# Optimization experiments

Measured on AMD Instinct MI355X. Metric: run time of the kernel, lower is better.

Reference implementation:

```python
import jax, jax.numpy as jnp
import numpy as np

EMBED = 1024
HEADS = 16
HEAD_DIM = EMBED // HEADS


def setup_inputs() -> dict:
    key = jax.random.key(0)
    k1, k2, k3 = jax.random.split(key, 3)
    hidden_states = jax.random.normal(k1, (2, 2048, EMBED), dtype=jnp.float32)
    # Conv1D weights are stored (nx, nf): y = x @ W + b
    c_attn_w = jax.random.normal(k2, (EMBED, 3 * EMBED), dtype=jnp.float32) * 0.02
    c_attn_b = jnp.zeros((3 * EMBED,), dtype=jnp.float32)
    c_proj_w = jax.random.normal(k3, (EMBED, EMBED), dtype=jnp.float32) * 0.02
    c_proj_b = jnp.zeros((EMBED,), dtype=jnp.float32)
    return {
        "hidden_states": hidden_states,
        "c_attn_w": c_attn_w,
        "c_attn_b": c_attn_b,
        "c_proj_w": c_proj_w,
        "c_proj_b": c_proj_b,
    }


def reference(hidden_states, c_attn_w, c_attn_b, c_proj_w, c_proj_b):
    B, S, E = hidden_states.shape
    H, D = HEADS, HEAD_DIM
    fused = hidden_states @ c_attn_w + c_attn_b  # [B,S,3E]
    q, k, v = jnp.split(fused, 3, axis=-1)
    # split heads -> [B,H,S,D]
    q = q.reshape(B, S, H, D).transpose(0, 2, 1, 3)
    k = k.reshape(B, S, H, D).transpose(0, 2, 1, 3)
    v = v.reshape(B, S, H, D).transpose(0, 2, 1, 3)
    scores = jnp.einsum("bhqd,bhkd->bhqk", q, k) / jnp.sqrt(jnp.float32(D))
    probs = jax.nn.softmax(scores, axis=-1)  # NOTE: no causal mask in source
    attn = jnp.einsum("bhqk,bhkd->bhqd", probs, v)
    out = attn.transpose(0, 2, 1, 3).reshape(B, S, E)
    return out @ c_proj_w + c_proj_b
```

## Files before the change

kernel.cpp:

```cpp
#include <hip/hip_runtime.h>
#include <hip/hip_bf16.h>
#include <cstdint>
#include <cstddef>

#define E_ 1024
#define H_ 16
#define D_ 64
#define B_ 2
#define S_ 2048
#define T_ 4096
#define NQ_ 3072

typedef __bf16 bf16_t;
typedef bf16_t bf16x8 __attribute__((ext_vector_type(8)));
typedef float f32x4 __attribute__((ext_vector_type(4)));

static __device__ __forceinline__ unsigned short f2bf(float f) {
    __hip_bfloat16 h = __float2bfloat16(f);
    return __builtin_bit_cast(unsigned short, h);
}
static __device__ __forceinline__ unsigned pack2(float a, float b) {
    return (unsigned)f2bf(a) | ((unsigned)f2bf(b) << 16);
}
static __device__ __forceinline__ bf16x8 ld_frag(const unsigned short* p) {
    uint4 u = *reinterpret_cast<const uint4*>(p);
    return __builtin_bit_cast(bf16x8, u);
}
static __device__ __forceinline__ void cp16(unsigned short* lds, const unsigned short* g) {
    __builtin_amdgcn_global_load_lds(
        (const __attribute__((address_space(1))) unsigned int*)g,
        (__attribute__((address_space(3))) unsigned int*)lds, 16, 0, 0);
}
static __device__ __forceinline__ f32x4 mfma16(bf16x8 a, bf16x8 b, f32x4 c) {
    return __builtin_amdgcn_mfma_f32_16x16x32_bf16(a, b, c, 0, 0, 0);
}
static __device__ __forceinline__ unsigned pack2_trunc(unsigned a_bits, unsigned b_bits) {
    return __builtin_amdgcn_perm(b_bits, a_bits, 0x07060302u);
}


__global__ __launch_bounds__(256) void k_cvt(const float* __restrict__ in,
                                             unsigned short* __restrict__ out, int n) {
    int i = (blockIdx.x * 256 + threadIdx.x) * 4;
    if (i < n) {
        float4 v = *reinterpret_cast<const float4*>(in + i);
        int tok = i >> 10, e = i & 1023;
        size_t off = ((size_t)(tok >> 7) * 32 + (e >> 5)) * 4096 + (tok & 127) * 32 + (e & 31);
        uint2 o;
        o.x = pack2(v.x, v.y);
        o.y = pack2(v.z, v.w);
        *reinterpret_cast<uint2*>(out + off) = o;
    }
}

__global__ __launch_bounds__(256) void k_wt(const float* __restrict__ in,
                                            unsigned short* __restrict__ out, int K, int N) {
    __shared__ float t[32][33];
    int n0 = blockIdx.x * 32, k0 = blockIdx.y * 32;
    int tx = threadIdx.x, ty = threadIdx.y;
    for (int j = 0; j < 4; j++) {
        int r = ty + j * 8;
        t[r][tx] = in[(size_t)(k0 + r) * N + n0 + tx];
    }
    __syncthreads();
    int nkt = K >> 5;
    for (int j = 0; j < 4; j++) {
        int r = ty + j * 8;
        int nn = n0 + r;
        size_t off = ((size_t)(nn >> 7) * nkt + (k0 >> 5)) * 4096 + (nn & 127) * 32 + tx;
        out[off] = f2bf(t[tx][r]);
    }
}

template <bool TR>
static __device__ __forceinline__ void gemm_tile_128(
    const unsigned short* __restrict__ At,
    const unsigned short* __restrict__ Bt,
    int nkt, int m0, int n0,
    unsigned short* As, unsigned short* Bs,
    f32x4 acc[4][4])
{
    const int t = threadIdx.x;
    const int w = t >> 6, lane = t & 63, lr = lane & 15, lq = lane >> 4;
    const int wm = (w >> 1) * 64, wn = (w & 1) * 64;
    for (int mt = 0; mt < 4; mt++)
        for (int nt = 0; nt < 4; nt++)
            acc[mt][nt] = (f32x4){0.f, 0.f, 0.f, 0.f};

    const unsigned short* ag = At + (size_t)(m0 >> 7) * nkt * 4096 + t * 8;
    const unsigned short* bg = Bt + (size_t)(n0 >> 7) * nkt * 4096 + t * 8;

    for (int kt = 0; kt < nkt; kt++) {
        __syncthreads();
        cp16(&As[t * 8], ag);          cp16(&As[(t + 256) * 8], ag + 2048);
        cp16(&Bs[t * 8], bg);          cp16(&Bs[(t + 256) * 8], bg + 2048);
        ag += 4096; bg += 4096;
        __syncthreads();
        bf16x8 af[4], bfr[4];
        for (int mt = 0; mt < 4; mt++) af[mt]  = ld_frag(&As[(wm + mt * 16 + lr) * 32 + lq * 8]);
        for (int nt = 0; nt < 4; nt++) bfr[nt] = ld_frag(&Bs[(wn + nt * 16 + lr) * 32 + lq * 8]);
        for (int mt = 0; mt < 4; mt++)
            for (int nt = 0; nt < 4; nt++)
                acc[mt][nt] = TR ? mfma16(bfr[nt], af[mt], acc[mt][nt])
                                 : mfma16(af[mt], bfr[nt], acc[mt][nt]);
    }
}

__global__ __launch_bounds__(256) void k_qkv(
    const unsigned short* __restrict__ Ab, const unsigned short* __restrict__ Wt,
    const float* __restrict__ bias,
    unsigned short* __restrict__ Qb, unsigned short* __restrict__ Kimg,
    unsigned short* __restrict__ Vimg)
{
    __shared__ __attribute__((aligned(16))) unsigned short As[128 * 32];
    __shared__ __attribute__((aligned(16))) unsigned short Bs[128 * 32];
    f32x4 acc[4][4];
    int m0 = blockIdx.x * 128, n0 = blockIdx.y * 128;
    int sector = (n0 >> 10);
    if (sector == 2) gemm_tile_128<false>(Ab, Wt, E_ / 32, m0, n0, As, Bs, acc);
    else             gemm_tile_128<true >(Ab, Wt, E_ / 32, m0, n0, As, Bs, acc);

    int t = threadIdx.x, w = t >> 6, lane = t & 63, lr = lane & 15, lq = lane >> 4;
    int wm = (w >> 1) * 64, wn = (w & 1) * 64;

    if (sector == 2) {
        for (int nt = 0; nt < 4; nt++) {
            int n = n0 + wn + nt * 16 + lr;
            float bv = bias[n];
            int nn = n & 1023, hh = nn >> 6, d = nn & 63;
            for (int mt = 0; mt < 4; mt++) {
                int tok0 = m0 + wm + mt * 16 + lq * 4;
                int bb = tok0 >> 11, s0 = tok0 & 2047;
                size_t headOff = (size_t)(bb * H_ + hh) * (S_ * D_);
                int tile = s0 >> 7, j = s0 & 127, stripe = j >> 5, lq_ = (j >> 3) & 3, pos = j & 7;
                int dt = d >> 4;
                size_t off = headOff + (size_t)tile * 8192 +
                    ((size_t)((stripe * 4 + dt) * 64 + lq_ * 16 + (d & 15))) * 8 + pos;
                uint2 u;
                u.x = pack2(acc[mt][nt][0] + bv, acc[mt][nt][1] + bv);
                u.y = pack2(acc[mt][nt][2] + bv, acc[mt][nt][3] + bv);
                *reinterpret_cast<uint2*>(Vimg + off) = u;
            }
        }
    } else {
        for (int nt = 0; nt < 4; nt++) {
            int n = n0 + wn + nt * 16 + lq * 4;
            float4 bv4 = *reinterpret_cast<const float4*>(&bias[n]);
            int nn = n & 1023, hh = nn >> 6, d0 = nn & 63;
            for (int mt = 0; mt < 4; mt++) {
                int tok = m0 + wm + mt * 16 + lr;
                int bb = tok >> 11, s = tok & 2047;
                size_t headOff = (size_t)(bb * H_ + hh) * (S_ * D_);
                float v0 = acc[mt][nt][0] + bv4.x, v1 = acc[mt][nt][1] + bv4.y;
                float v2 = acc[mt][nt][2] + bv4.z, v3 = acc[mt][nt][3] + bv4.w;
                if (sector == 0) {
                    const float c = 0.18033688011112042f;
                    uint2 u;
                    u.x = pack2(v0 * c, v1 * c);
                    u.y = pack2(v2 * c, v3 * c);
                    *reinterpret_cast<uint2*>(Qb + headOff + (size_t)s * 64 + d0) = u;
                } else {
                    int dc = d0 >> 5, lq_ = (d0 >> 3) & 3, pos = d0 & 7;
                    int tile = s >> 7, j = s & 127, stripe = j >> 5, jj = j & 31;
                    int h2 = (jj >> 2) & 1, slot = ((jj >> 3) << 2) | (jj & 3);
                    size_t off = headOff + (size_t)tile * 8192 +
                        ((size_t)(((stripe * 2 + h2) * 2 + dc) * 64 + lq_ * 16 + slot)) * 8 + pos;
                    uint2 u;
                    u.x = pack2(v0, v1);
                    u.y = pack2(v2, v3);
                    *reinterpret_cast<uint2*>(Kimg + off) = u;
                }
            }
        }
    }
}

__global__ __launch_bounds__(256) void k_attn(
    const unsigned short* __restrict__ Qb, const unsigned short* __restrict__ Kimg,
    const unsigned short* __restrict__ Vimg, unsigned short* __restrict__ Ao)
{
    __shared__ __attribute__((aligned(16))) unsigned short smem[16896];
    unsigned short* Ks = smem;
    unsigned short* Vt = smem + 8192;
    float* Lred = (float*)(smem + 16384);
    float* Ored = (float*)smem;

    const int t = threadIdx.x, w = t >> 6, lane = t & 63, lr = lane & 15, lq = lane >> 4;

    const int id = blockIdx.x;
    const int xcd = id & 7, slot = id >> 3;
    const int qblk = slot & 31;
    const int hb = ((slot >> 5) << 3) | xcd;
    const int h = hb & 15, b = hb >> 4;

    const size_t head = (size_t)(b * H_ + h) * (S_ * D_);
    const unsigned short* Qh = Qb + head;
    const unsigned short* kg = Kimg + head + t * 8;
    const unsigned short* vg = Vimg + head + t * 8;
    const int q0 = qblk * 64;

    bf16x8 qf[4][2];
    for (int qt = 0; qt < 4; qt++)
        for (int dc = 0; dc < 2; dc++)
            qf[qt][dc] = ld_frag(&Qh[(size_t)(q0 + qt * 16 + lr) * 64 + dc * 32 + lq * 8]);

    bf16x8 ones;
    {
        uint4 u = {0x3f803f80u, 0x3f803f80u, 0x3f803f80u, 0x3f803f80u};
        ones = __builtin_bit_cast(bf16x8, u);
    }

    f32x4 o[4][4];
    f32x4 oL[4];
    for (int qt = 0; qt < 4; qt++) {
        oL[qt] = (f32x4){0.f, 0.f, 0.f, 0.f};
        for (int dt = 0; dt < 4; dt++)
            o[qt][dt] = (f32x4){0.f, 0.f, 0.f, 0.f};
    }

    for (int it = 0; it < S_ / 128; it++) {
        __syncthreads();
        cp16(&Ks[t * 8], kg);                cp16(&Ks[(t + 256) * 8], kg + 2048);
        cp16(&Ks[(t + 512) * 8], kg + 4096); cp16(&Ks[(t + 768) * 8], kg + 6144);
        cp16(&Vt[t * 8], vg);                cp16(&Vt[(t + 256) * 8], vg + 2048);
        cp16(&Vt[(t + 512) * 8], vg + 4096); cp16(&Vt[(t + 768) * 8], vg + 6144);
        kg += 8192; vg += 8192;
        __syncthreads();

        f32x4 z[2][4];
#pragma unroll
        for (int h2 = 0; h2 < 2; h2++) {
            bf16x8 kf0 = ld_frag(&Ks[((w * 4 + h2 * 2 + 0) * 64 + lane) * 8]);
            bf16x8 kf1 = ld_frag(&Ks[((w * 4 + h2 * 2 + 1) * 64 + lane) * 8]);
            for (int qt = 0; qt < 4; qt++) {
                f32x4 zz = (f32x4){0.f, 0.f, 0.f, 0.f};
                zz = mfma16(kf0, qf[qt][0], zz);
                zz = mfma16(kf1, qf[qt][1], zz);
                z[h2][qt] = zz;
            }
        }
        bf16x8 pb[4];
#pragma unroll
        for (int qt = 0; qt < 4; qt++) {
            unsigned e0 = __builtin_bit_cast(unsigned, __builtin_amdgcn_exp2f(z[0][qt][0]));
            unsigned e1 = __builtin_bit_cast(unsigned, __builtin_amdgcn_exp2f(z[0][qt][1]));
            unsigned e2 = __builtin_bit_cast(unsigned, __builtin_amdgcn_exp2f(z[0][qt][2]));
            unsigned e3 = __builtin_bit_cast(unsigned, __builtin_amdgcn_exp2f(z[0][qt][3]));
            unsigned e4 = __builtin_bit_cast(unsigned, __builtin_amdgcn_exp2f(z[1][qt][0]));
            unsigned e5 = __builtin_bit_cast(unsigned, __builtin_amdgcn_exp2f(z[1][qt][1]));
            unsigned e6 = __builtin_bit_cast(unsigned, __builtin_amdgcn_exp2f(z[1][qt][2]));
            unsigned e7 = __builtin_bit_cast(unsigned, __builtin_amdgcn_exp2f(z[1][qt][3]));
            uint4 u;
            u.x = pack2_trunc(e0, e1);
            u.y = pack2_trunc(e2, e3);
            u.z = pack2_trunc(e4, e5);
            u.w = pack2_trunc(e6, e7);
            pb[qt] = __builtin_bit_cast(bf16x8, u);
        }
        for (int qt = 0; qt < 4; qt++)
            oL[qt] = mfma16(ones, pb[qt], oL[qt]);
        bf16x8 vf[4];
#pragma unroll
        for (int dt = 0; dt < 4; dt++)
            vf[dt] = ld_frag(&Vt[((w * 4 + dt) * 64 + lane) * 8]);
        for (int qt = 0; qt < 4; qt++)
            for (int dt = 0; dt < 4; dt++)
                o[qt][dt] = mfma16(vf[dt], pb[qt], o[qt][dt]);
    }

    __syncthreads();

    if (lq == 0)
        for (int qt = 0; qt < 4; qt++)
            Lred[w * 64 + qt * 16 + lr] = oL[qt][0];

    for (int ww = 0; ww < 4; ww++) {
        if (w == ww) {
            for (int qt = 0; qt < 4; qt++)
                for (int dt = 0; dt < 4; dt++) {
                    int q = qt * 16 + lr, d = dt * 16 + lq * 4;
                    float4* p = reinterpret_cast<float4*>(&Ored[q * 68 + d]);
                    float4 vv = {o[qt][dt][0], o[qt][dt][1], o[qt][dt][2], o[qt][dt][3]};
                    if (ww == 0) *p = vv;
                    else {
                        float4 c = *p;
                        c.x += vv.x; c.y += vv.y; c.z += vv.z; c.w += vv.w;
                        *p = c;
                    }
                }
        }
        __syncthreads();
    }

    {
        int q = t >> 2, dsg = (t & 3) * 16;
        float inv = 1.0f / (Lred[q] + Lred[64 + q] + Lred[128 + q] + Lred[192 + q]);
        const float* rp = &Ored[q * 68 + dsg];
        unsigned u[8];
        for (int j = 0; j < 8; j++)
            u[j] = pack2(rp[2 * j] * inv, rp[2 * j + 1] * inv);
        int tok = b * S_ + q0 + q, e = h * 64 + dsg;
        size_t off = ((size_t)(tok >> 7) * 32 + (e >> 5)) * 4096 + (tok & 127) * 32 + (e & 31);
        uint4 s0 = {u[0], u[1], u[2], u[3]};
        uint4 s1 = {u[4], u[5], u[6], u[7]};
        *reinterpret_cast<uint4*>(&Ao[off]) = s0;
        *reinterpret_cast<uint4*>(&Ao[off + 8]) = s1;
    }
}

__global__ __launch_bounds__(256) void k_proj(
    const unsigned short* __restrict__ Ab, const unsigned short* __restrict__ Wt,
    const float* __restrict__ bias, float* __restrict__ out)
{
    __shared__ __attribute__((aligned(16))) unsigned short As[128 * 32];
    __shared__ __attribute__((aligned(16))) unsigned short Bs[128 * 32];
    f32x4 acc[4][4];
    int m0 = blockIdx.x * 128, n0 = blockIdx.y * 128;
    gemm_tile_128<true>(Ab, Wt, E_ / 32, m0, n0, As, Bs, acc);

    int t = threadIdx.x, w = t >> 6, lane = t & 63, lr = lane & 15, lq = lane >> 4;
    int wm = (w >> 1) * 64, wn = (w & 1) * 64;
    for (int nt = 0; nt < 4; nt++) {
        int n = n0 + wn + nt * 16 + lq * 4;
        float4 bv4 = *reinterpret_cast<const float4*>(&bias[n]);
        for (int mt = 0; mt < 4; mt++) {
            int tok = m0 + wm + mt * 16 + lr;
            float4 vv = {acc[mt][nt][0] + bv4.x, acc[mt][nt][1] + bv4.y,
                         acc[mt][nt][2] + bv4.z, acc[mt][nt][3] + bv4.w};
            *reinterpret_cast<float4*>(&out[(size_t)tok * E_ + n]) = vv;
        }
    }
}

extern "C" void kernel_launch(void* const* d_in, const int* in_sizes, int n_in,
                              void* d_out, int out_size, void* d_ws, size_t ws_size,
                              hipStream_t stream) {
    const float* hs = (const float*)d_in[0];
    const float* w1 = (const float*)d_in[1];
    const float* b1 = (const float*)d_in[2];
    const float* w2 = (const float*)d_in[3];
    const float* b2 = (const float*)d_in[4];
    float* out = (float*)d_out;

    char* ws = (char*)d_ws;
    unsigned short* hb  = (unsigned short*)(ws);
    unsigned short* w1t = (unsigned short*)(ws + (size_t)( 8 << 20));
    unsigned short* w2t = (unsigned short*)(ws + (size_t)(14 << 20));
    unsigned short* Qb  = (unsigned short*)(ws + (size_t)(16 << 20));
    unsigned short* Kim = (unsigned short*)(ws + (size_t)(24 << 20));
    unsigned short* Vim = (unsigned short*)(ws + (size_t)(32 << 20));
    unsigned short* Ao  = (unsigned short*)(ws + (size_t)(40 << 20));

    k_cvt<<<dim3(T_ * E_ / 1024), dim3(256), 0, stream>>>(hs, hb, T_ * E_);
    k_wt<<<dim3(NQ_ / 32, E_ / 32), dim3(32, 8), 0, stream>>>(w1, w1t, E_, NQ_);
    k_wt<<<dim3(E_ / 32, E_ / 32), dim3(32, 8), 0, stream>>>(w2, w2t, E_, E_);
    k_qkv<<<dim3(T_ / 128, NQ_ / 128), dim3(256), 0, stream>>>(hb, w1t, b1, Qb, Kim, Vim);
    k_attn<<<dim3(S_ / 64 * H_ * B_), dim3(256), 0, stream>>>(Qb, Kim, Vim, Ao);
    k_proj<<<dim3(T_ / 128, E_ / 128), dim3(256), 0, stream>>>(Ao, w2t, b2, out);
}
```

Measured before the change: 218.6 us.

## Double-buffer GEMM and attention LDS tiles, fuse prep kernels, swizzle fragment layout

Merges the three preprocessing kernels (activation conversion and both weight transposes) into one launch. Reorders the bf16 tile layout so each wave's MFMA fragment is a contiguous 64-lane × 16-byte block in LDS, avoiding strided fragment reads. Double-buffers the LDS tiles in the GEMM and attention K/V loops so the next tile's async global→LDS copy overlaps the current tile's MFMAs, with one barrier per iteration instead of two. The cost is twice the LDS per block (64KB in attention), which may lower occupancy.

```diff
diff --git a/kernel.cpp b/kernel.cpp
--- a/kernel.cpp
+++ b/kernel.cpp
@@ -39,36 +39,51 @@
 }
 
 
-__global__ __launch_bounds__(256) void k_cvt(const float* __restrict__ in,
-                                             unsigned short* __restrict__ out, int n) {
-    int i = (blockIdx.x * 256 + threadIdx.x) * 4;
-    if (i < n) {
-        float4 v = *reinterpret_cast<const float4*>(in + i);
+__global__ __launch_bounds__(256) void k_pre(const float* __restrict__ hs,
+                                             const float* __restrict__ w1,
+                                             const float* __restrict__ w2,
+                                             unsigned short* __restrict__ hb,
+                                             unsigned short* __restrict__ w1t,
+                                             unsigned short* __restrict__ w2t) {
+    __shared__ float tsh[32][33];
+    int id = blockIdx.x, t = threadIdx.x;
+    if (id < 4096) {
+        int i = (id * 256 + t) * 4;
+        float4 v = *reinterpret_cast<const float4*>(hs + i);
         int tok = i >> 10, e = i & 1023;
-        size_t off = ((size_t)(tok >> 7) * 32 + (e >> 5)) * 4096 + (tok & 127) * 32 + (e & 31);
+        int p = ((tok & 127) >> 4) * 64 + ((e & 31) >> 3) * 16 + (tok & 15);
+        size_t off = ((size_t)(tok >> 7) * 32 + (e >> 5)) * 4096 + p * 8 + (e & 7);
         uint2 o;
         o.x = pack2(v.x, v.y);
         o.y = pack2(v.z, v.w);
-        *reinterpret_cast<uint2*>(out + off) = o;
-    }
-}
-
-__global__ __launch_bounds__(256) void k_wt(const float* __restrict__ in,
-                                            unsigned short* __restrict__ out, int K, int N) {
-    __shared__ float t[32][33];
-    int n0 = blockIdx.x * 32, k0 = blockIdx.y * 32;
-    int tx = threadIdx.x, ty = threadIdx.y;
-    for (int j = 0; j < 4; j++) {
-        int r = ty + j * 8;
-        t[r][tx] = in[(size_t)(k0 + r) * N + n0 + tx];
-    }
-    __syncthreads();
-    int nkt = K >> 5;
-    for (int j = 0; j < 4; j++) {
-        int r = ty + j * 8;
-        int nn = n0 + r;
-        size_t off = ((size_t)(nn >> 7) * nkt + (k0 >> 5)) * 4096 + (nn & 127) * 32 + tx;
-        out[off] = f2bf(t[tx][r]);
+        *reinterpret_cast<uint2*>(hb + off) = o;
+    } else {
+        const float* in;
+        unsigned short* out;
+        int bx, by, N, nkt;
+        if (id < 4096 + 3072) {
+            int bid = id - 4096;
+            in = w1; out = w1t; N = NQ_; nkt = 32;
+            bx = bid % 96; by = bid / 96;
+        } else {
+            int bid = id - 7168;
+            in = w2; out = w2t; N = E_; nkt = 32;
+            bx = bid & 31; by = bid >> 5;
+        }
+        int n0 = bx * 32, k0 = by * 32;
+        int tx = t & 31, ty = t >> 5;
+        for (int j = 0; j < 4; j++) {
+            int r = ty + j * 8;
+            tsh[r][tx] = in[(size_t)(k0 + r) * N + n0 + tx];
+        }
+        __syncthreads();
+        for (int j = 0; j < 4; j++) {
+            int r = ty + j * 8;
+            int nn = n0 + r;
+            int p = ((nn & 127) >> 4) * 64 + (tx >> 3) * 16 + (nn & 15);
+            size_t off = ((size_t)(nn >> 7) * nkt + (k0 >> 5)) * 4096 + p * 8 + (tx & 7);
+            out[off] = f2bf(tsh[tx][r]);
+        }
     }
 }
 
@@ -81,8 +96,8 @@
     f32x4 acc[4][4])
 {
     const int t = threadIdx.x;
-    const int w = t >> 6, lane = t & 63, lr = lane & 15, lq = lane >> 4;
-    const int wm = (w >> 1) * 64, wn = (w & 1) * 64;
+    const int w = t >> 6, lane = t & 63;
+    const int wmg = (w >> 1) * 4, wng = (w & 1) * 4;
     for (int mt = 0; mt < 4; mt++)
         for (int nt = 0; nt < 4; nt++)
             acc[mt][nt] = (f32x4){0.f, 0.f, 0.f, 0.f};
@@ -90,19 +105,29 @@
     const unsigned short* ag = At + (size_t)(m0 >> 7) * nkt * 4096 + t * 8;
     const unsigned short* bg = Bt + (size_t)(n0 >> 7) * nkt * 4096 + t * 8;
 
+    cp16(&As[t * 8], ag);  cp16(&As[(t + 256) * 8], ag + 2048);
+    cp16(&Bs[t * 8], bg);  cp16(&Bs[(t + 256) * 8], bg + 2048);
+    ag += 4096; bg += 4096;
+    __syncthreads();
+
     for (int kt = 0; kt < nkt; kt++) {
-        __syncthreads();
-        cp16(&As[t * 8], ag);          cp16(&As[(t + 256) * 8], ag + 2048);
-        cp16(&Bs[t * 8], bg);          cp16(&Bs[(t + 256) * 8], bg + 2048);
-        ag += 4096; bg += 4096;
-        __syncthreads();
+        unsigned short* Ap = As + (kt & 1) * 4096;
+        unsigned short* Bp = Bs + (kt & 1) * 4096;
+        if (kt + 1 < nkt) {
+            unsigned short* An = As + ((kt + 1) & 1) * 4096;
+            unsigned short* Bn = Bs + ((kt + 1) & 1) * 4096;
+            cp16(&An[t * 8], ag);  cp16(&An[(t + 256) * 8], ag + 2048);
+            cp16(&Bn[t * 8], bg);  cp16(&Bn[(t + 256) * 8], bg + 2048);
+            ag += 4096; bg += 4096;
+        }
         bf16x8 af[4], bfr[4];
-        for (int mt = 0; mt < 4; mt++) af[mt]  = ld_frag(&As[(wm + mt * 16 + lr) * 32 + lq * 8]);
-        for (int nt = 0; nt < 4; nt++) bfr[nt] = ld_frag(&Bs[(wn + nt * 16 + lr) * 32 + lq * 8]);
+        for (int mt = 0; mt < 4; mt++) af[mt]  = ld_frag(&Ap[((wmg + mt) * 64 + lane) * 8]);
+        for (int nt = 0; nt < 4; nt++) bfr[nt] = ld_frag(&Bp[((wng + nt) * 64 + lane) * 8]);
         for (int mt = 0; mt < 4; mt++)
             for (int nt = 0; nt < 4; nt++)
                 acc[mt][nt] = TR ? mfma16(bfr[nt], af[mt], acc[mt][nt])
                                  : mfma16(af[mt], bfr[nt], acc[mt][nt]);
+        __syncthreads();
     }
 }
 
@@ -112,8 +137,8 @@
     unsigned short* __restrict__ Qb, unsigned short* __restrict__ Kimg,
     unsigned short* __restrict__ Vimg)
 {
-    __shared__ __attribute__((aligned(16))) unsigned short As[128 * 32];
-    __shared__ __attribute__((aligned(16))) unsigned short Bs[128 * 32];
+    __shared__ __attribute__((aligned(16))) unsigned short As[2 * 4096];
+    __shared__ __attribute__((aligned(16))) unsigned short Bs[2 * 4096];
     f32x4 acc[4][4];
     int m0 = blockIdx.x * 128, n0 = blockIdx.y * 128;
     int sector = (n0 >> 10);
@@ -179,10 +204,8 @@
     const unsigned short* __restrict__ Qb, const unsigned short* __restrict__ Kimg,
     const unsigned short* __restrict__ Vimg, unsigned short* __restrict__ Ao)
 {
-    __shared__ __attribute__((aligned(16))) unsigned short smem[16896];
-    unsigned short* Ks = smem;
-    unsigned short* Vt = smem + 8192;
-    float* Lred = (float*)(smem + 16384);
+    __shared__ __attribute__((aligned(16))) unsigned short smem[32768];
+    float* Lred = (float*)(smem + 28672);
     float* Ored = (float*)smem;
 
     const int t = threadIdx.x, w = t >> 6, lane = t & 63, lr = lane & 15, lq = lane >> 4;
@@ -218,14 +241,29 @@
             o[qt][dt] = (f32x4){0.f, 0.f, 0.f, 0.f};
     }
 
+    {
+        unsigned short* K0 = smem;
+        unsigned short* V0 = smem + 16384;
+        cp16(&K0[t * 8], kg);                cp16(&K0[(t + 256) * 8], kg + 2048);
+        cp16(&K0[(t + 512) * 8], kg + 4096); cp16(&K0[(t + 768) * 8], kg + 6144);
+        cp16(&V0[t * 8], vg);                cp16(&V0[(t + 256) * 8], vg + 2048);
+        cp16(&V0[(t + 512) * 8], vg + 4096); cp16(&V0[(t + 768) * 8], vg + 6144);
+        kg += 8192; vg += 8192;
+    }
+    __syncthreads();
+
     for (int it = 0; it < S_ / 128; it++) {
-        __syncthreads();
-        cp16(&Ks[t * 8], kg);                cp16(&Ks[(t + 256) * 8], kg + 2048);
-        cp16(&Ks[(t + 512) * 8], kg + 4096); cp16(&Ks[(t + 768) * 8], kg + 6144);
-        cp16(&Vt[t * 8], vg);                cp16(&Vt[(t + 256) * 8], vg + 2048);
-        cp16(&Vt[(t + 512) * 8], vg + 4096); cp16(&Vt[(t + 768) * 8], vg + 6144);
-        kg += 8192; vg += 8192;
-        __syncthreads();
+        unsigned short* Ks = smem + (it & 1) * 8192;
+        unsigned short* Vt = smem + 16384 + (it & 1) * 8192;
+        if (it + 1 < S_ / 128) {
+            unsigned short* Kn = smem + ((it + 1) & 1) * 8192;
+            unsigned short* Vn = smem + 16384 + ((it + 1) & 1) * 8192;
+            cp16(&Kn[t * 8], kg);                cp16(&Kn[(t + 256) * 8], kg + 2048);
+            cp16(&Kn[(t + 512) * 8], kg + 4096); cp16(&Kn[(t + 768) * 8], kg + 6144);
+            cp16(&Vn[t * 8], vg);                cp16(&Vn[(t + 256) * 8], vg + 2048);
+            cp16(&Vn[(t + 512) * 8], vg + 4096); cp16(&Vn[(t + 768) * 8], vg + 6144);
+            kg += 8192; vg += 8192;
+        }
 
         f32x4 z[2][4];
 #pragma unroll
@@ -266,9 +304,9 @@
         for (int qt = 0; qt < 4; qt++)
             for (int dt = 0; dt < 4; dt++)
                 o[qt][dt] = mfma16(vf[dt], pb[qt], o[qt][dt]);
-    }
-
-    __syncthreads();
+
+        __syncthreads();
+    }
 
     if (lq == 0)
         for (int qt = 0; qt < 4; qt++)
@@ -299,12 +337,13 @@
         unsigned u[8];
         for (int j = 0; j < 8; j++)
             u[j] = pack2(rp[2 * j] * inv, rp[2 * j + 1] * inv);
-        int tok = b * S_ + q0 + q, e = h * 64 + dsg;
-        size_t off = ((size_t)(tok >> 7) * 32 + (e >> 5)) * 4096 + (tok & 127) * 32 + (e & 31);
+        int tok = b * S_ + q0 + q, e0 = h * 64 + dsg;
+        int p = ((tok & 127) >> 4) * 64 + ((e0 & 31) >> 3) * 16 + (tok & 15);
+        size_t base = ((size_t)(tok >> 7) * 32 + (e0 >> 5)) * 4096;
         uint4 s0 = {u[0], u[1], u[2], u[3]};
         uint4 s1 = {u[4], u[5], u[6], u[7]};
-        *reinterpret_cast<uint4*>(&Ao[off]) = s0;
-        *reinterpret_cast<uint4*>(&Ao[off + 8]) = s1;
+        *reinterpret_cast<uint4*>(&Ao[base + p * 8]) = s0;
+        *reinterpret_cast<uint4*>(&Ao[base + (p + 16) * 8]) = s1;
     }
 }
 
@@ -312,8 +351,8 @@
     const unsigned short* __restrict__ Ab, const unsigned short* __restrict__ Wt,
     const float* __restrict__ bias, float* __restrict__ out)
 {
-    __shared__ __attribute__((aligned(16))) unsigned short As[128 * 32];
-    __shared__ __attribute__((aligned(16))) unsigned short Bs[128 * 32];
+    __shared__ __attribute__((aligned(16))) unsigned short As[2 * 4096];
+    __shared__ __attribute__((aligned(16))) unsigned short Bs[2 * 4096];
     f32x4 acc[4][4];
     int m0 = blockIdx.x * 128, n0 = blockIdx.y * 128;
     gemm_tile_128<true>(Ab, Wt, E_ / 32, m0, n0, As, Bs, acc);
@@ -351,9 +390,7 @@
     unsigned short* Vim = (unsigned short*)(ws + (size_t)(32 << 20));
     unsigned short* Ao  = (unsigned short*)(ws + (size_t)(40 << 20));
 
-    k_cvt<<<dim3(T_ * E_ / 1024), dim3(256), 0, stream>>>(hs, hb, T_ * E_);
-    k_wt<<<dim3(NQ_ / 32, E_ / 32), dim3(32, 8), 0, stream>>>(w1, w1t, E_, NQ_);
-    k_wt<<<dim3(E_ / 32, E_ / 32), dim3(32, 8), 0, stream>>>(w2, w2t, E_, E_);
+    k_pre<<<dim3(4096 + 3072 + 1024), dim3(256), 0, stream>>>(hs, w1, w2, hb, w1t, w2t);
     k_qkv<<<dim3(T_ / 128, NQ_ / 128), dim3(256), 0, stream>>>(hb, w1t, b1, Qb, Kim, Vim);
     k_attn<<<dim3(S_ / 64 * H_ * B_), dim3(256), 0, stream>>>(Qb, Kim, Vim, Ao);
     k_proj<<<dim3(T_ / 128, E_ / 128), dim3(256), 0, stream>>>(Ao, w2t, b2, out);
```

After: 228.8 us. 4.7% more time.
